# Kernel optimization log

Hardware: AMD Instinct MI355X
Metric: run time of the kernel (lower is better)

The kernel has to match this reference:

```python
import jax, jax.numpy as jnp
import numpy as np

FP8_MAX = 448.0


def _quantize_fp8(x):
    """Per-tensor symmetric quantization matching the Triton kernel's decode.

    Encode: u = round(clip(x*scale, -448, 448) / 448 * 127)  (stored as u+128 in uint8)
    Decode: x_hat = u / 127 * 448 / scale,  with scale = 448 / amax(|x|).
    We keep u as a float array of integers in [-127, 127] (the +128 uint8 bias
    cancels in the kernel's `u - 128`).
    """
    amax = jnp.max(jnp.abs(x))
    scale = FP8_MAX / jnp.maximum(amax, jnp.asarray(1e-12, x.dtype))
    q = jnp.clip(x * scale, -FP8_MAX, FP8_MAX)
    u = jnp.round(q / FP8_MAX * 127.0)
    return u, scale


def reference(x, weight):
    orig_shape = x.shape
    K = weight.shape[1]
    x2d = x.reshape(-1, K)                      # [M, K]

    ua, a_scale = _quantize_fp8(x2d)            # codes + per-tensor scale
    uw, w_scale = _quantize_fp8(weight)         # weight: [N, K]

    # Kernel dequant: val = u / 127 * FP8_MAX; acc in fp32; rescale by 1/(a_scale*b_scale)
    a_f = ua * (FP8_MAX / 127.0)
    b_f = (uw * (FP8_MAX / 127.0)).T            # [K, N] (weight_fp8.t())
    acc = a_f @ b_f                              # fp32 accumulate, [M, N]
    out = acc * (1.0 / (a_scale * w_scale))
    out = out.astype(x.dtype)
    return out.reshape(*orig_shape[:-1], weight.shape[0])


def setup_inputs() -> dict:
    key = jax.random.key(0)
    k1, k2 = jax.random.split(key)
    x = jax.random.normal(k1, (4, 2048, 4096), dtype=jnp.float32)
    weight = jax.random.normal(k2, (8192, 4096), dtype=jnp.float32) * 0.02
    return {"x": x, "weight": weight}
```

## Files before the change

### kernel.cpp

```cpp
#include <hip/hip_runtime.h>

#define FP8_MAX_F 448.0f

static constexpr int M = 8192;
static constexpr int N = 8192;
static constexpr int K = 4096;

typedef __attribute__((ext_vector_type(4))) int i32x4;

#define AS1 __attribute__((address_space(1)))
#define AS3 __attribute__((address_space(3)))
#define BARRIER() asm volatile("s_barrier" ::: "memory")
#define VMCNT(n)  asm volatile("s_waitcnt vmcnt(" #n ")" ::: "memory")

__global__ void amax_kernel(const float* __restrict__ x, const float* __restrict__ w,
                            unsigned* __restrict__ out) {
    const long n4x = (long)M * K / 4;
    const long n4t = n4x + (long)N * K / 4;
    unsigned lx = 0u, lw = 0u;
    const long stride = (long)gridDim.x * blockDim.x;
    for (long i = (long)blockIdx.x * blockDim.x + threadIdx.x; i < n4t; i += stride) {
        if (i < n4x) {
            float4 v = ((const float4*)x)[i];
            unsigned a0 = __float_as_uint(v.x) & 0x7fffffffu;
            unsigned a1 = __float_as_uint(v.y) & 0x7fffffffu;
            unsigned a2 = __float_as_uint(v.z) & 0x7fffffffu;
            unsigned a3 = __float_as_uint(v.w) & 0x7fffffffu;
            lx = max(lx, max(max(a0, a1), max(a2, a3)));
        } else {
            float4 v = ((const float4*)w)[i - n4x];
            unsigned a0 = __float_as_uint(v.x) & 0x7fffffffu;
            unsigned a1 = __float_as_uint(v.y) & 0x7fffffffu;
            unsigned a2 = __float_as_uint(v.z) & 0x7fffffffu;
            unsigned a3 = __float_as_uint(v.w) & 0x7fffffffu;
            lw = max(lw, max(max(a0, a1), max(a2, a3)));
        }
    }
    #pragma unroll
    for (int off = 32; off > 0; off >>= 1) {
        lx = max(lx, (unsigned)__shfl_down((int)lx, off, 64));
        lw = max(lw, (unsigned)__shfl_down((int)lw, off, 64));
    }
    __shared__ unsigned smx[4], smw[4];
    if ((threadIdx.x & 63) == 0) { smx[threadIdx.x >> 6] = lx; smw[threadIdx.x >> 6] = lw; }
    __syncthreads();
    if (threadIdx.x == 0) {
        atomicMax(&out[0], max(max(smx[0], smx[1]), max(smx[2], smx[3])));
        atomicMax(&out[1], max(max(smw[0], smw[1]), max(smw[2], smw[3])));
    }
}

__device__ __forceinline__ signed char quant1(float v, float s) {
    float f = fminf(fmaxf(v * s, -FP8_MAX_F), FP8_MAX_F);
    return (signed char)(int)rintf(f / FP8_MAX_F * 127.0f);
}

__global__ void quant_kernel(const float* __restrict__ x, const float* __restrict__ w,
                             signed char* __restrict__ qx, signed char* __restrict__ qw,
                             const unsigned* __restrict__ amax_bits) {
    const float ax = fmaxf(__uint_as_float(amax_bits[0]), 1e-12f);
    const float aw = fmaxf(__uint_as_float(amax_bits[1]), 1e-12f);
    const float sxv = FP8_MAX_F / ax;
    const float swv = FP8_MAX_F / aw;
    const long cx = (long)M * K / 16;
    const long ct = cx + (long)N * K / 16;
    const long stride = (long)gridDim.x * blockDim.x;
    for (long ci = (long)blockIdx.x * blockDim.x + threadIdx.x; ci < ct; ci += stride) {
        const float* src; signed char* dst; float s; long c;
        if (ci < cx) { src = x; dst = qx; s = sxv; c = ci; }
        else         { src = w; dst = qw; s = swv; c = ci - cx; }
        const long r = c >> 8;
        const int  cr = (int)(c & 255);
        const float4* in = (const float4*)(src + r * K + cr * 16);
        signed char ob[16];
        #pragma unroll
        for (int j = 0; j < 4; ++j) {
            float4 v = in[j];
            ob[j * 4 + 0] = quant1(v.x, s);
            ob[j * 4 + 1] = quant1(v.y, s);
            ob[j * 4 + 2] = quant1(v.z, s);
            ob[j * 4 + 3] = quant1(v.w, s);
        }
        const int osub = (cr & 3) ^ ((int)(r >> 1) & 3);
        *(int4*)(dst + r * K + ((long)((cr & ~3) + osub)) * 16) = *(const int4*)ob;
    }
}

__global__ __launch_bounds__(512, 2) void gemm_i8_kernel(
    const signed char* __restrict__ Aq, const signed char* __restrict__ Bq,
    float* __restrict__ C, const unsigned* __restrict__ amax_bits)
{
    __shared__ signed char lds[4][2][256 * 64];

    const int tid  = threadIdx.x;
    const int wid  = tid >> 6;
    const int lane = tid & 63;
    const int wm = wid >> 2;
    const int wn = wid & 3;
    const int fr = lane & 15;
    const int fq = lane >> 4;

    const long row0 = (long)blockIdx.x * 256;
    const long col0 = (long)blockIdx.y * 256;
    const signed char* Ablk = Aq + row0 * K;
    const signed char* Bblk = Bq + col0 * K;

    const long stag_off = (long)(tid >> 2) * K + (long)(tid & 3) * 16;

    const int arow = wm * 128 + fr;
    const int aoff = arow * 64 + ((fq ^ ((arow >> 1) & 3)) * 16);
    const int brow = wn * 64 + fr;
    const int boff = brow * 64 + ((fq ^ ((brow >> 1) & 3)) * 16);

    i32x4 acc[8][4] = {};
    i32x4 afR[2][8];
    i32x4 bR[2][4];

#define STAGE_A(st, bi) do { \
        const signed char* g = Ablk + (long)(st) * 64 + stag_off; \
        __builtin_amdgcn_global_load_lds((const AS1 void*)g, \
            (AS3 void*)(&lds[bi][0][0] + wid * 1024), 16, 0, 0); \
        __builtin_amdgcn_global_load_lds((const AS1 void*)(g + 128L * K), \
            (AS3 void*)(&lds[bi][0][0] + 8192 + wid * 1024), 16, 0, 0); \
    } while (0)

#define STAGE_B(st, bi) do { \
        const signed char* g = Bblk + (long)(st) * 64 + stag_off; \
        __builtin_amdgcn_global_load_lds((const AS1 void*)g, \
            (AS3 void*)(&lds[bi][1][0] + wid * 1024), 16, 0, 0); \
        __builtin_amdgcn_global_load_lds((const AS1 void*)(g + 128L * K), \
            (AS3 void*)(&lds[bi][1][0] + 8192 + wid * 1024), 16, 0, 0); \
    } while (0)

    STAGE_A(0, 0); STAGE_B(0, 0);
    STAGE_A(1, 1); STAGE_B(1, 1);
    STAGE_A(2, 2); STAGE_B(2, 2);
    VMCNT(4);
    BARRIER();
    #pragma unroll
    for (int mi = 0; mi < 8; ++mi)
        afR[0][mi] = *(const i32x4*)(&lds[0][0][0] + aoff + mi * 1024);
    #pragma unroll
    for (int ni = 0; ni < 4; ++ni)
        bR[0][ni] = *(const i32x4*)(&lds[0][1][0] + boff + ni * 1024);

#define TILE_BODY(t, CUR, NXT) do { \
        const signed char* la = &lds[((t) + 1) & 3][0][0]; \
        const signed char* lb = &lds[((t) + 1) & 3][1][0]; \
        _Pragma("unroll") \
        for (int mi = 0; mi < 8; ++mi) \
            afR[NXT][mi] = *(const i32x4*)(la + aoff + mi * 1024); \
        STAGE_A(((t) + 3) & 63, ((t) + 3) & 3); \
        BARRIER(); \
        __builtin_amdgcn_s_setprio(1); \
        _Pragma("unroll") \
        for (int mi = 0; mi < 8; ++mi) { \
            acc[mi][0] = __builtin_amdgcn_mfma_i32_16x16x64_i8(afR[CUR][mi], bR[CUR][0], acc[mi][0], 0, 0, 0); \
            acc[mi][1] = __builtin_amdgcn_mfma_i32_16x16x64_i8(afR[CUR][mi], bR[CUR][1], acc[mi][1], 0, 0, 0); \
        } \
        __builtin_amdgcn_s_setprio(0); \
        BARRIER(); \
        _Pragma("unroll") \
        for (int ni = 0; ni < 4; ++ni) \
            bR[NXT][ni] = *(const i32x4*)(lb + boff + ni * 1024); \
        STAGE_B(((t) + 3) & 63, ((t) + 3) & 3); \
        VMCNT(4); \
        BARRIER(); \
        __builtin_amdgcn_s_setprio(1); \
        _Pragma("unroll") \
        for (int mi = 0; mi < 8; ++mi) { \
            acc[mi][2] = __builtin_amdgcn_mfma_i32_16x16x64_i8(afR[CUR][mi], bR[CUR][2], acc[mi][2], 0, 0, 0); \
            acc[mi][3] = __builtin_amdgcn_mfma_i32_16x16x64_i8(afR[CUR][mi], bR[CUR][3], acc[mi][3], 0, 0, 0); \
        } \
        __builtin_amdgcn_s_setprio(0); \
        BARRIER(); \
    } while (0)

    #pragma unroll 1
    for (int t = 0; t < 64; t += 2) {
        TILE_BODY(t, 0, 1);
        TILE_BODY(t + 1, 1, 0);
    }

#undef TILE_BODY
#undef STAGE_B
#undef STAGE_A

    const float ax = fmaxf(__uint_as_float(amax_bits[0]), 1e-12f);
    const float aw = fmaxf(__uint_as_float(amax_bits[1]), 1e-12f);
    const float factor = ax * aw * (1.0f / (127.0f * 127.0f));

    #pragma unroll
    for (int mi = 0; mi < 8; ++mi) {
        #pragma unroll
        for (int ni = 0; ni < 4; ++ni) {
            const long col = col0 + wn * 64 + ni * 16 + fr;
            #pragma unroll
            for (int j = 0; j < 4; ++j) {
                const long row = row0 + wm * 128 + mi * 16 + fq * 4 + j;
                C[row * N + col] = (float)acc[mi][ni][j] * factor;
            }
        }
    }
}

extern "C" void kernel_launch(void* const* d_in, const int* in_sizes, int n_in,
                              void* d_out, int out_size, void* d_ws, size_t ws_size,
                              hipStream_t stream) {
    const float* x = (const float*)d_in[0];
    const float* w = (const float*)d_in[1];
    float* out = (float*)d_out;

    unsigned char* ws = (unsigned char*)d_ws;
    unsigned* amax = (unsigned*)ws;
    signed char* aq = (signed char*)(ws + 256);
    signed char* wq = aq + (long)M * K;

    hipMemsetAsync(amax, 0, 2 * sizeof(unsigned), stream);
    amax_kernel<<<2048, 256, 0, stream>>>(x, w, amax);
    quant_kernel<<<4096, 256, 0, stream>>>(x, w, aq, wq, amax);

    dim3 grid(M / 256, N / 256);
    gemm_i8_kernel<<<grid, 512, 0, stream>>>(aq, wq, out, amax);
}
```

Measured before the change: 419.4 us.

## Restructure GEMM main loop into single-phase stages with swizzled block order

The int8 GEMM main loop now does all LDS reads (A and B) for the next tile, then issues one combined A+B global-to-LDS stage, then runs all 32 MFMAs between barriers. This replaces the previous two half-phases that split the B fragments and the A/B staging. The prologue and epilogue are rewritten explicitly so the loop no longer loads past K, which drops the old modulo-64 wrap-around prefetch. The grid becomes 1D with an XCD-style swizzle of block ids, which aims to improve L2 reuse of A/B tiles across concurrently running blocks. The trade-off is fewer barriers per tile and longer MFMA runs, against less interleaving of LDS reads and staging with compute.

```diff
diff --git a/kernel.cpp b/kernel.cpp
--- a/kernel.cpp
+++ b/kernel.cpp
@@ -100,8 +100,11 @@
     const int fr = lane & 15;
     const int fq = lane >> 4;
 
-    const long row0 = (long)blockIdx.x * 256;
-    const long col0 = (long)blockIdx.y * 256;
+    const int bid = blockIdx.x;
+    const int swz = (bid & 7) * 128 + (bid >> 3);
+    const long row0 = (long)(swz & 31) * 256;
+    const long col0 = (long)(swz >> 5) * 256;
+
     const signed char* Ablk = Aq + row0 * K;
     const signed char* Bblk = Bq + col0 * K;
 
@@ -116,75 +119,71 @@
     i32x4 afR[2][8];
     i32x4 bR[2][4];
 
-#define STAGE_A(st, bi) do { \
-        const signed char* g = Ablk + (long)(st) * 64 + stag_off; \
-        __builtin_amdgcn_global_load_lds((const AS1 void*)g, \
-            (AS3 void*)(&lds[bi][0][0] + wid * 1024), 16, 0, 0); \
-        __builtin_amdgcn_global_load_lds((const AS1 void*)(g + 128L * K), \
-            (AS3 void*)(&lds[bi][0][0] + 8192 + wid * 1024), 16, 0, 0); \
+#define STAGE_AB(st) do { \
+        const signed char* ga = Ablk + (long)(st) * 64 + stag_off; \
+        const signed char* gb = Bblk + (long)(st) * 64 + stag_off; \
+        signed char* lA = &lds[(st) & 3][0][0]; \
+        signed char* lB = &lds[(st) & 3][1][0]; \
+        __builtin_amdgcn_global_load_lds((const AS1 void*)ga, \
+            (AS3 void*)(lA + wid * 1024), 16, 0, 0); \
+        __builtin_amdgcn_global_load_lds((const AS1 void*)(ga + 128L * K), \
+            (AS3 void*)(lA + 8192 + wid * 1024), 16, 0, 0); \
+        __builtin_amdgcn_global_load_lds((const AS1 void*)gb, \
+            (AS3 void*)(lB + wid * 1024), 16, 0, 0); \
+        __builtin_amdgcn_global_load_lds((const AS1 void*)(gb + 128L * K), \
+            (AS3 void*)(lB + 8192 + wid * 1024), 16, 0, 0); \
     } while (0)
 
-#define STAGE_B(st, bi) do { \
-        const signed char* g = Bblk + (long)(st) * 64 + stag_off; \
-        __builtin_amdgcn_global_load_lds((const AS1 void*)g, \
-            (AS3 void*)(&lds[bi][1][0] + wid * 1024), 16, 0, 0); \
-        __builtin_amdgcn_global_load_lds((const AS1 void*)(g + 128L * K), \
-            (AS3 void*)(&lds[bi][1][0] + 8192 + wid * 1024), 16, 0, 0); \
-    } while (0)
-
-    STAGE_A(0, 0); STAGE_B(0, 0);
-    STAGE_A(1, 1); STAGE_B(1, 1);
-    STAGE_A(2, 2); STAGE_B(2, 2);
-    VMCNT(4);
-    BARRIER();
-    #pragma unroll
-    for (int mi = 0; mi < 8; ++mi)
-        afR[0][mi] = *(const i32x4*)(&lds[0][0][0] + aoff + mi * 1024);
-    #pragma unroll
-    for (int ni = 0; ni < 4; ++ni)
-        bR[0][ni] = *(const i32x4*)(&lds[0][1][0] + boff + ni * 1024);
-
-#define TILE_BODY(t, CUR, NXT) do { \
-        const signed char* la = &lds[((t) + 1) & 3][0][0]; \
-        const signed char* lb = &lds[((t) + 1) & 3][1][0]; \
+#define READS(t1, NXT) do { \
+        const signed char* la = &lds[(t1) & 3][0][0]; \
+        const signed char* lb = &lds[(t1) & 3][1][0]; \
         _Pragma("unroll") \
         for (int mi = 0; mi < 8; ++mi) \
             afR[NXT][mi] = *(const i32x4*)(la + aoff + mi * 1024); \
-        STAGE_A(((t) + 3) & 63, ((t) + 3) & 3); \
+        _Pragma("unroll") \
+        for (int ni = 0; ni < 4; ++ni) \
+            bR[NXT][ni] = *(const i32x4*)(lb + boff + ni * 1024); \
+    } while (0)
+
+#define MFMA32(CUR) do { \
         BARRIER(); \
         __builtin_amdgcn_s_setprio(1); \
         _Pragma("unroll") \
         for (int mi = 0; mi < 8; ++mi) { \
-            acc[mi][0] = __builtin_amdgcn_mfma_i32_16x16x64_i8(afR[CUR][mi], bR[CUR][0], acc[mi][0], 0, 0, 0); \
-            acc[mi][1] = __builtin_amdgcn_mfma_i32_16x16x64_i8(afR[CUR][mi], bR[CUR][1], acc[mi][1], 0, 0, 0); \
-        } \
-        __builtin_amdgcn_s_setprio(0); \
-        BARRIER(); \
-        _Pragma("unroll") \
-        for (int ni = 0; ni < 4; ++ni) \
-            bR[NXT][ni] = *(const i32x4*)(lb + boff + ni * 1024); \
-        STAGE_B(((t) + 3) & 63, ((t) + 3) & 3); \
-        VMCNT(4); \
-        BARRIER(); \
-        __builtin_amdgcn_s_setprio(1); \
-        _Pragma("unroll") \
-        for (int mi = 0; mi < 8; ++mi) { \
-            acc[mi][2] = __builtin_amdgcn_mfma_i32_16x16x64_i8(afR[CUR][mi], bR[CUR][2], acc[mi][2], 0, 0, 0); \
-            acc[mi][3] = __builtin_amdgcn_mfma_i32_16x16x64_i8(afR[CUR][mi], bR[CUR][3], acc[mi][3], 0, 0, 0); \
+            _Pragma("unroll") \
+            for (int ni = 0; ni < 4; ++ni) \
+                acc[mi][ni] = __builtin_amdgcn_mfma_i32_16x16x64_i8( \
+                    afR[CUR][mi], bR[CUR][ni], acc[mi][ni], 0, 0, 0); \
         } \
         __builtin_amdgcn_s_setprio(0); \
         BARRIER(); \
     } while (0)
 
+    STAGE_AB(0); STAGE_AB(1); STAGE_AB(2);
+    VMCNT(4);
+    BARRIER();
+    READS(0, 0);
+
     #pragma unroll 1
-    for (int t = 0; t < 64; t += 2) {
-        TILE_BODY(t, 0, 1);
-        TILE_BODY(t + 1, 1, 0);
-    }
-
-#undef TILE_BODY
-#undef STAGE_B
-#undef STAGE_A
+    for (int t = 0; t < 60; t += 2) {
+        READS(t + 1, 1);
+        STAGE_AB(t + 3);
+        VMCNT(4);
+        MFMA32(0);
+
+        READS(t + 2, 0);
+        STAGE_AB(t + 4);
+        VMCNT(4);
+        MFMA32(1);
+    }
+    READS(61, 1); STAGE_AB(63); VMCNT(4); MFMA32(0);
+    READS(62, 0);               VMCNT(0); MFMA32(1);
+    READS(63, 1);                         MFMA32(0);
+    MFMA32(1);
+
+#undef MFMA32
+#undef READS
+#undef STAGE_AB
 
     const float ax = fmaxf(__uint_as_float(amax_bits[0]), 1e-12f);
     const float aw = fmaxf(__uint_as_float(amax_bits[1]), 1e-12f);
@@ -220,6 +219,5 @@
     amax_kernel<<<2048, 256, 0, stream>>>(x, w, amax);
     quant_kernel<<<4096, 256, 0, stream>>>(x, w, aq, wq, amax);
 
-    dim3 grid(M / 256, N / 256);
-    gemm_i8_kernel<<<grid, 512, 0, stream>>>(aq, wq, out, amax);
-}
+    gemm_i8_kernel<<<1024, 512, 0, stream>>>(aq, wq, out, amax);
+}
```

After: 539.0 us. 28.5% more time.
